# Kernel optimization log

Measured on AMD Instinct MI355X. Metric: run time of the kernel, lower is better.

The kernel has to match this reference:

```python
import jax, jax.numpy as jnp
import numpy as np

N1, N2, F = 512, 512, 128
H = 512  # hidden width


def _xavier(key, shape):
    fan_in, fan_out = shape
    std = (2.0 / (fan_in + fan_out)) ** 0.5
    return jax.random.normal(key, shape, dtype=jnp.float32) * std


def setup_inputs() -> dict:
    key = jax.random.key(0)
    ks = jax.random.split(key, 8)
    V1 = jax.random.normal(ks[0], (1, N1, F), dtype=jnp.float32)
    V2 = jax.random.normal(ks[1], (1, N2, F), dtype=jnp.float32)
    W1 = _xavier(ks[2], (2 * F, H))
    b1 = 0.0001 + 5e-05 * jax.random.normal(ks[3], (H,), dtype=jnp.float32)
    W2 = _xavier(ks[4], (H, H))
    b2 = 0.0001 + 5e-05 * jax.random.normal(ks[5], (H,), dtype=jnp.float32)
    W3 = _xavier(ks[6], (H, 2))
    b3 = 0.0001 + 5e-05 * jax.random.normal(ks[7], (2,), dtype=jnp.float32)
    return {"V1": V1, "V2": V2, "W1": W1, "b1": b1, "W2": W2, "b2": b2, "W3": W3, "b3": b3}


def reference(V1, V2, W1, b1, W2, b2, W3, b3):
    n1, n2, f = V1.shape[1], V2.shape[1], V1.shape[2]
    # Fused broadcast-concat replacing the N1*N2 Python double loop
    # (i outer, j inner; V1[i] first, V2[j] second -> row-major reshape matches stack order)
    pairs = jnp.concatenate([
        jnp.broadcast_to(V1[0][:, None, :], (n1, n2, f)),
        jnp.broadcast_to(V2[0][None, :, :], (n1, n2, f)),
    ], axis=-1).reshape(1, n1 * n2, 2 * f)
    h = jax.nn.relu(pairs @ W1 + b1)
    h = jax.nn.relu(h @ W2 + b2)
    out = jax.nn.relu(h @ W3 + b3)  # final LinearEmbedding also has ReLU by default
    return out
```

## Files before the change

kernel.cpp:

```cpp
#include <hip/hip_runtime.h>


typedef short bf16x8 __attribute__((ext_vector_type(8)));
typedef float f32x16 __attribute__((ext_vector_type(16)));

#define NROW 512
#define FDIM 128
#define HDIM 512

__device__ __forceinline__ unsigned int pk2(float x, float y) {
  unsigned int r;
  asm("v_cvt_pk_bf16_f32 %0, %1, %2" : "=v"(r) : "v"(x), "v"(y));
  return r;
}
__device__ __forceinline__ unsigned short f2bf(float x) {
  unsigned int u = __builtin_bit_cast(unsigned int, x);
  u += 0x7fffu + ((u >> 16) & 1u);
  return (unsigned short)(u >> 16);
}
__device__ __forceinline__ float bflo(unsigned int u) {
  return __builtin_bit_cast(float, u << 16);
}
__device__ __forceinline__ float bfhi(unsigned int u) {
  return __builtin_bit_cast(float, u & 0xffff0000u);
}

__global__ __launch_bounds__(256) void prep_ab(
    const float* __restrict__ V1, const float* __restrict__ V2,
    const float* __restrict__ W1, const float* __restrict__ b1,
    float* __restrict__ Ap, unsigned short* __restrict__ Bpb) {
  __shared__ float sv[4 * FDIM];
  const int b = blockIdx.x;
  const int t = threadIdx.x;
  const bool isB = b >= 128;
  const int r0 = (b & 127) * 4;
  const float* V = isB ? V2 : V1;
  const float* W = W1 + (isB ? FDIM * HDIM : 0);
  for (int idx = t; idx < 4 * FDIM; idx += 256) sv[idx] = V[r0 * FDIM + idx];
  __syncthreads();
  float s[4][2] = {};
  for (int k = 0; k < FDIM; ++k) {
    const float w0 = W[k * HDIM + t];
    const float w1 = W[k * HDIM + t + 256];
#pragma unroll
    for (int r = 0; r < 4; ++r) {
      const float v = sv[r * FDIM + k];
      s[r][0] += v * w0;
      s[r][1] += v * w1;
    }
  }
  if (isB) {
#pragma unroll
    for (int r = 0; r < 4; ++r) {
      Bpb[(r0 + r) * HDIM + t] = f2bf(s[r][0]);
      Bpb[(r0 + r) * HDIM + t + 256] = f2bf(s[r][1]);
    }
  } else {
    const float bb0 = b1[t];
    const float bb1 = b1[t + 256];
#pragma unroll
    for (int r = 0; r < 4; ++r) {
      Ap[(r0 + r) * HDIM + t] = s[r][0] + bb0;
      Ap[(r0 + r) * HDIM + t + 256] = s[r][1] + bb1;
    }
  }
}

__global__ __launch_bounds__(256) void prep_w2(const float* __restrict__ W2,
                                               unsigned short* __restrict__ W2T) {
  const int o = blockIdx.x * 256 + threadIdx.x;
  const int kc = o >> 9;
  const int n = o & 511;
  unsigned int u[4];
#pragma unroll
  for (int e2 = 0; e2 < 4; ++e2)
    u[e2] = pk2(W2[(kc * 8 + 2 * e2) * HDIM + n], W2[(kc * 8 + 2 * e2 + 1) * HDIM + n]);
  *(uint4*)(W2T + (size_t)o * 8) = make_uint4(u[0], u[1], u[2], u[3]);
}

__global__ __launch_bounds__(512, 2) void mlp_main(
    const float* __restrict__ Ap, const unsigned short* __restrict__ Bpb,
    const unsigned short* __restrict__ W2T, const float* __restrict__ b2,
    const float* __restrict__ W3, const float* __restrict__ b3,
    float* __restrict__ out) {
  extern __shared__ char smem[];
  char* sA = smem;

  const int tid = threadIdx.x;
  const int wave = tid >> 6;
  const int lane = tid & 63;
  const int cl = lane & 31;
  const int hi = lane >> 5;
  const int r15 = lane & 15;

  const int m0 = blockIdx.x * 128;
  const int i = m0 >> 9;
  const int j0 = m0 & 511;

  const char* bbase = (const char*)W2T + (((wave << 6) + cl) << 4) + (hi << 13);

  bf16x8 af[2][4], bfr[5][2];
#pragma unroll
  for (int q = 0; q < 4; ++q) {
    const char* bp = bbase + ((size_t)q << 14);
    bfr[q][0] = *(const bf16x8*)(bp);
    bfr[q][1] = *(const bf16x8*)(bp + (1 << 9));
  }
  float w30[2], w31[2], bb[2];
#pragma unroll
  for (int nt = 0; nt < 2; ++nt) {
    const int n = (wave << 6) + (nt << 5) + cl;
    w30[nt] = W3[2 * n];
    w31[nt] = W3[2 * n + 1];
    bb[nt] = b2[n];
  }
  const float bb3_0 = b3[0], bb3_1 = b3[1];

  {
    const int c = tid & 63;
    const int rsub = tid >> 6;
    const float4 a0 = *(const float4*)(Ap + i * HDIM + c * 8);
    const float4 a1 = *(const float4*)(Ap + i * HDIM + c * 8 + 4);
#pragma unroll
    for (int it = 0; it < 16; ++it) {
      const int row = it * 8 + rsub;
      const uint4 ub = *(const uint4*)(Bpb + (size_t)(j0 + row) * HDIM + c * 8);
      const uint4 v = make_uint4(
          pk2(fmaxf(a0.x + bflo(ub.x), 0.f), fmaxf(a0.y + bfhi(ub.x), 0.f)),
          pk2(fmaxf(a0.z + bflo(ub.y), 0.f), fmaxf(a0.w + bfhi(ub.y), 0.f)),
          pk2(fmaxf(a1.x + bflo(ub.z), 0.f), fmaxf(a1.y + bfhi(ub.z), 0.f)),
          pk2(fmaxf(a1.z + bflo(ub.w), 0.f), fmaxf(a1.w + bfhi(ub.w), 0.f)));
      *(uint4*)(sA + row * 1024 + ((c ^ (row & 15)) << 4)) = v;
    }
  }
  __syncthreads();

  f32x16 acc[4][2];
#pragma unroll
  for (int mt = 0; mt < 4; ++mt)
#pragma unroll
    for (int nt = 0; nt < 2; ++nt)
#pragma unroll
      for (int q = 0; q < 16; ++q) acc[mt][nt][q] = 0.f;

  const char* abase0 = sA + cl * 1024;
  {
    const int off = (hi ^ r15) << 4;
#pragma unroll
    for (int mt = 0; mt < 4; ++mt) af[0][mt] = *(const bf16x8*)(abase0 + mt * 32768 + off);
  }
#pragma unroll
  for (int s = 0; s < 32; ++s) {
    const int cur = s & 1;
    if (s < 31) {
      const int off = ((((s + 1) << 1) | hi) ^ r15) << 4;
#pragma unroll
      for (int mt = 0; mt < 4; ++mt)
        af[cur ^ 1][mt] = *(const bf16x8*)(abase0 + mt * 32768 + off);
    }
    if (s < 28) {
      const char* bp = bbase + ((size_t)(s + 4) << 14);
      bfr[(s + 4) % 5][0] = *(const bf16x8*)(bp);
      bfr[(s + 4) % 5][1] = *(const bf16x8*)(bp + (1 << 9));
    }
    __builtin_amdgcn_s_setprio(1);
#pragma unroll
    for (int nt = 0; nt < 2; ++nt)
#pragma unroll
      for (int mt = 0; mt < 4; ++mt)
        acc[mt][nt] = __builtin_amdgcn_mfma_f32_32x32x16_bf16(af[cur][mt], bfr[s % 5][nt],
                                                              acc[mt][nt], 0, 0, 0);
    __builtin_amdgcn_s_setprio(0);
  }

  __syncthreads();

#pragma unroll
  for (int rnd = 0; rnd < 2; ++rnd) {
#pragma unroll
    for (int ml = 0; ml < 2; ++ml) {
      const int mt = rnd * 2 + ml;
      char* ebuf = smem + ml * 65536;
#pragma unroll
      for (int rp = 0; rp < 8; ++rp) {
        const int ra = 2 * rp;
        const float h0a = fmaxf(acc[mt][0][ra] + bb[0], 0.f);
        const float h1a = fmaxf(acc[mt][1][ra] + bb[1], 0.f);
        const float h0b = fmaxf(acc[mt][0][ra + 1] + bb[0], 0.f);
        const float h1b = fmaxf(acc[mt][1][ra + 1] + bb[1], 0.f);
        const float4 v =
            make_float4(h0a * w30[0] + h1a * w30[1], h0a * w31[0] + h1a * w31[1],
                        h0b * w30[0] + h1b * w30[1], h0b * w31[0] + h1b * w31[1]);
        const int rpi = ((ra & 3) + 8 * (ra >> 2) + 4 * hi) >> 1;
        *(float4*)(ebuf + rpi * 4096 + (((wave << 5) + cl) << 4)) = v;
      }
    }
    __syncthreads();
    {
      const int ml = tid >> 8;
      const int t2 = tid & 255;
      const int rpi = t2 >> 4;
      const int sub = t2 & 15;
      const char* ebuf = smem + ml * 65536;
      float4 s4 = make_float4(0.f, 0.f, 0.f, 0.f);
#pragma unroll
      for (int k = 0; k < 16; ++k) {
        const float4 v = *(const float4*)(ebuf + rpi * 4096 + ((sub + (k << 4)) << 4));
        s4.x += v.x; s4.y += v.y; s4.z += v.z; s4.w += v.w;
      }
#pragma unroll
      for (int d = 1; d < 16; d <<= 1) {
        s4.x += __shfl_xor(s4.x, d, 64);
        s4.y += __shfl_xor(s4.y, d, 64);
        s4.z += __shfl_xor(s4.z, d, 64);
        s4.w += __shfl_xor(s4.w, d, 64);
      }
      if (sub == 0) {
        const int rg = m0 + ((rnd * 2 + ml) << 5) + (rpi << 1);
        *(float4*)(out + rg * 2) =
            make_float4(fmaxf(s4.x + bb3_0, 0.f), fmaxf(s4.y + bb3_1, 0.f),
                        fmaxf(s4.z + bb3_0, 0.f), fmaxf(s4.w + bb3_1, 0.f));
      }
    }
    __syncthreads();
  }
}

extern "C" void kernel_launch(void* const* d_in, const int* in_sizes, int n_in,
                              void* d_out, int out_size, void* d_ws, size_t ws_size,
                              hipStream_t stream) {
  const float* V1 = (const float*)d_in[0];
  const float* V2 = (const float*)d_in[1];
  const float* W1 = (const float*)d_in[2];
  const float* b1 = (const float*)d_in[3];
  const float* W2 = (const float*)d_in[4];
  const float* b2 = (const float*)d_in[5];
  const float* W3 = (const float*)d_in[6];
  const float* b3 = (const float*)d_in[7];

  float* Ap = (float*)d_ws;
  unsigned short* Bpb = (unsigned short*)(Ap + NROW * HDIM);
  unsigned short* W2T = Bpb + NROW * HDIM;

  const int smem_bytes = 131072;
  (void)hipFuncSetAttribute((const void*)mlp_main,
                            hipFuncAttributeMaxDynamicSharedMemorySize, smem_bytes);

  prep_ab<<<256, 256, 0, stream>>>(V1, V2, W1, b1, Ap, Bpb);
  prep_w2<<<128, 256, 0, stream>>>(W2, W2T);
  mlp_main<<<2048, 512, smem_bytes, stream>>>(Ap, Bpb, W2T, b2, W3, b3, (float*)d_out);
}
```

Before: 144.9 us.

## Split N across 16 waves with 1024-thread blocks and single N tile per wave

```diff
diff --git a/kernel.cpp b/kernel.cpp
--- a/kernel.cpp
+++ b/kernel.cpp
@@ -78,7 +78,7 @@
   *(uint4*)(W2T + (size_t)o * 8) = make_uint4(u[0], u[1], u[2], u[3]);
 }
 
-__global__ __launch_bounds__(512, 2) void mlp_main(
+__global__ __launch_bounds__(1024, 4) void mlp_main(
     const float* __restrict__ Ap, const unsigned short* __restrict__ Bpb,
     const unsigned short* __restrict__ W2T, const float* __restrict__ b2,
     const float* __restrict__ W3, const float* __restrict__ b3,
@@ -97,23 +97,16 @@
   const int i = m0 >> 9;
   const int j0 = m0 & 511;
 
-  const char* bbase = (const char*)W2T + (((wave << 6) + cl) << 4) + (hi << 13);
-
-  bf16x8 af[2][4], bfr[5][2];
-#pragma unroll
-  for (int q = 0; q < 4; ++q) {
-    const char* bp = bbase + ((size_t)q << 14);
-    bfr[q][0] = *(const bf16x8*)(bp);
-    bfr[q][1] = *(const bf16x8*)(bp + (1 << 9));
-  }
-  float w30[2], w31[2], bb[2];
-#pragma unroll
-  for (int nt = 0; nt < 2; ++nt) {
-    const int n = (wave << 6) + (nt << 5) + cl;
-    w30[nt] = W3[2 * n];
-    w31[nt] = W3[2 * n + 1];
-    bb[nt] = b2[n];
-  }
+  const char* bbase = (const char*)W2T + (((wave << 5) + cl) << 4) + (hi << 13);
+
+  bf16x8 af[2][4], bfr[3];
+#pragma unroll
+  for (int q = 0; q < 2; ++q) bfr[q] = *(const bf16x8*)(bbase + ((size_t)q << 14));
+
+  const int ncol = (wave << 5) + cl;
+  const float w30 = W3[2 * ncol];
+  const float w31 = W3[2 * ncol + 1];
+  const float bb = b2[ncol];
   const float bb3_0 = b3[0], bb3_1 = b3[1];
 
   {
@@ -122,8 +115,8 @@
     const float4 a0 = *(const float4*)(Ap + i * HDIM + c * 8);
     const float4 a1 = *(const float4*)(Ap + i * HDIM + c * 8 + 4);
 #pragma unroll
-    for (int it = 0; it < 16; ++it) {
-      const int row = it * 8 + rsub;
+    for (int it = 0; it < 8; ++it) {
+      const int row = it * 16 + rsub;
       const uint4 ub = *(const uint4*)(Bpb + (size_t)(j0 + row) * HDIM + c * 8);
       const uint4 v = make_uint4(
           pk2(fmaxf(a0.x + bflo(ub.x), 0.f), fmaxf(a0.y + bfhi(ub.x), 0.f)),
@@ -135,13 +128,11 @@
   }
   __syncthreads();
 
-  f32x16 acc[4][2];
+  f32x16 acc[4];
 #pragma unroll
   for (int mt = 0; mt < 4; ++mt)
 #pragma unroll
-    for (int nt = 0; nt < 2; ++nt)
-#pragma unroll
-      for (int q = 0; q < 16; ++q) acc[mt][nt][q] = 0.f;
+    for (int q = 0; q < 16; ++q) acc[mt][q] = 0.f;
 
   const char* abase0 = sA + cl * 1024;
   {
@@ -158,65 +149,46 @@
       for (int mt = 0; mt < 4; ++mt)
         af[cur ^ 1][mt] = *(const bf16x8*)(abase0 + mt * 32768 + off);
     }
-    if (s < 28) {
-      const char* bp = bbase + ((size_t)(s + 4) << 14);
-      bfr[(s + 4) % 5][0] = *(const bf16x8*)(bp);
-      bfr[(s + 4) % 5][1] = *(const bf16x8*)(bp + (1 << 9));
-    }
+    if (s < 30) bfr[(s + 2) % 3] = *(const bf16x8*)(bbase + ((size_t)(s + 2) << 14));
     __builtin_amdgcn_s_setprio(1);
 #pragma unroll
-    for (int nt = 0; nt < 2; ++nt)
-#pragma unroll
-      for (int mt = 0; mt < 4; ++mt)
-        acc[mt][nt] = __builtin_amdgcn_mfma_f32_32x32x16_bf16(af[cur][mt], bfr[s % 5][nt],
-                                                              acc[mt][nt], 0, 0, 0);
+    for (int mt = 0; mt < 4; ++mt)
+      acc[mt] = __builtin_amdgcn_mfma_f32_32x32x16_bf16(af[cur][mt], bfr[s % 3], acc[mt], 0, 0, 0);
     __builtin_amdgcn_s_setprio(0);
   }
 
   __syncthreads();
 
 #pragma unroll
-  for (int rnd = 0; rnd < 2; ++rnd) {
-#pragma unroll
-    for (int ml = 0; ml < 2; ++ml) {
-      const int mt = rnd * 2 + ml;
-      char* ebuf = smem + ml * 65536;
-#pragma unroll
-      for (int rp = 0; rp < 8; ++rp) {
-        const int ra = 2 * rp;
-        const float h0a = fmaxf(acc[mt][0][ra] + bb[0], 0.f);
-        const float h1a = fmaxf(acc[mt][1][ra] + bb[1], 0.f);
-        const float h0b = fmaxf(acc[mt][0][ra + 1] + bb[0], 0.f);
-        const float h1b = fmaxf(acc[mt][1][ra + 1] + bb[1], 0.f);
-        const float4 v =
-            make_float4(h0a * w30[0] + h1a * w30[1], h0a * w31[0] + h1a * w31[1],
-                        h0b * w30[0] + h1b * w30[1], h0b * w31[0] + h1b * w31[1]);
-        const int rpi = ((ra & 3) + 8 * (ra >> 2) + 4 * hi) >> 1;
-        *(float4*)(ebuf + rpi * 4096 + (((wave << 5) + cl) << 4)) = v;
-      }
+  for (int mt = 0; mt < 4; ++mt) {
+#pragma unroll
+    for (int rp = 0; rp < 8; ++rp) {
+      const int ra = 2 * rp;
+      const float h0a = fmaxf(acc[mt][ra] + bb, 0.f);
+      const float h0b = fmaxf(acc[mt][ra + 1] + bb, 0.f);
+      const float4 v = make_float4(h0a * w30, h0a * w31, h0b * w30, h0b * w31);
+      const int rpi = ((ra & 3) + 8 * (ra >> 2) + 4 * hi) >> 1;
+      *(float4*)(smem + rpi * 8192 + (((wave << 5) + cl) << 4)) = v;
     }
     __syncthreads();
     {
-      const int ml = tid >> 8;
-      const int t2 = tid & 255;
-      const int rpi = t2 >> 4;
-      const int sub = t2 & 15;
-      const char* ebuf = smem + ml * 65536;
+      const int rpi = tid >> 6;
+      const int sub = tid & 63;
       float4 s4 = make_float4(0.f, 0.f, 0.f, 0.f);
 #pragma unroll
-      for (int k = 0; k < 16; ++k) {
-        const float4 v = *(const float4*)(ebuf + rpi * 4096 + ((sub + (k << 4)) << 4));
+      for (int k = 0; k < 8; ++k) {
+        const float4 v = *(const float4*)(smem + rpi * 8192 + ((sub + (k << 6)) << 4));
         s4.x += v.x; s4.y += v.y; s4.z += v.z; s4.w += v.w;
       }
 #pragma unroll
-      for (int d = 1; d < 16; d <<= 1) {
+      for (int d = 1; d < 64; d <<= 1) {
         s4.x += __shfl_xor(s4.x, d, 64);
         s4.y += __shfl_xor(s4.y, d, 64);
         s4.z += __shfl_xor(s4.z, d, 64);
         s4.w += __shfl_xor(s4.w, d, 64);
       }
       if (sub == 0) {
-        const int rg = m0 + ((rnd * 2 + ml) << 5) + (rpi << 1);
+        const int rg = m0 + (mt << 5) + (rpi << 1);
         *(float4*)(out + rg * 2) =
             make_float4(fmaxf(s4.x + bb3_0, 0.f), fmaxf(s4.y + bb3_1, 0.f),
                         fmaxf(s4.z + bb3_0, 0.f), fmaxf(s4.w + bb3_1, 0.f));
@@ -248,5 +220,5 @@
 
   prep_ab<<<256, 256, 0, stream>>>(V1, V2, W1, b1, Ap, Bpb);
   prep_w2<<<128, 256, 0, stream>>>(W2, W2T);
-  mlp_main<<<2048, 512, smem_bytes, stream>>>(Ap, Bpb, W2T, b2, W3, b3, (float*)d_out);
-}
+  mlp_main<<<2048, 1024, smem_bytes, stream>>>(Ap, Bpb, W2T, b2, W3, b3, (float*)d_out);
+}
```

After: 191.3 us. +32.1%, slower.
